# Optimization experiments

Hardware: AMD Instinct MI355X
Metric: run time of the kernel (lower is better)

## Reference

```python
import jax, jax.numpy as jnp
import numpy as np


def _pad_kernel_like(kernel_oc0, H, W, ks):
    # torch: F.pad(k,(p,p,p,p)) then if shape mismatch F.pad(k,(0,1,0,1))
    p = (H - ks) // 2
    extra = H - (ks + 2 * p)  # 0 or 1
    return jnp.pad(kernel_oc0, ((0, 0), (p, p + extra), (p, p + extra)))


def setup_inputs() -> dict:
    key = jax.random.key(0)
    k1, k2 = jax.random.split(key)
    B, C, H, W = 8, 16, 128, 128
    O, KS = 32, 9
    x = jax.random.normal(k1, (B, C, H, W), dtype=jnp.float32)
    # kaiming_uniform-ish init scale
    fan_in = C * KS * KS
    bound = float(np.sqrt(6.0 / fan_in))
    kernel = jax.random.uniform(k2, (O, C, KS, KS), dtype=jnp.float32,
                                minval=-bound, maxval=bound)
    return {"x": x, "kernel": kernel}


def reference(x, kernel):
    # x: [B,C,H,W] float32, kernel: [O,C,ks,ks] float32
    B, C, H, W = x.shape
    O, ks = kernel.shape[0], kernel.shape[-1]
    # Faithful to original bug: only kernel[:, 0] is used for every input channel.
    k = _pad_kernel_like(kernel[:, 0], H, W, ks)  # [O,H,W]
    # 4f optical FFT convolution: ifftshift -> FFT -> multiply -> IFFT -> fftshift -> |.|
    Fx = jnp.fft.fft2(jnp.fft.ifftshift(x, axes=(-2, -1)))   # [B,C,H,W] complex64
    Fk = jnp.fft.fft2(jnp.fft.ifftshift(k, axes=(-2, -1)))   # [O,H,W]   complex64
    prod = Fx[:, None, :, :, :] * Fk[None, :, None, :, :]    # [B,O,C,H,W]
    field = jnp.fft.fftshift(jnp.fft.ifft2(prod), axes=(-2, -1))
    out_pc = jnp.abs(field)                                  # per-(out,in)-channel intensity
    return out_pc.sum(axis=2)                                # [B,O,H,W]
```

## Files before the change

### kernel.cpp

```cpp
#include <hip/hip_runtime.h>


typedef __attribute__((ext_vector_type(8)))  short  short8;
typedef __attribute__((ext_vector_type(4)))  float  float4v;
typedef __attribute__((ext_vector_type(4)))  unsigned int uint4v;

#define NROW 10
#define NCC  144
#define CHSZ (NROW * NCC)
#define NSLOT (16 * NROW * 72)

__device__ __forceinline__ unsigned short f2bf(float f) {
    union { float f; unsigned int u; } a; a.f = f;
    unsigned int u = a.u;
    u += 0x7fffu + ((u >> 16) & 1u);
    return (unsigned short)(u >> 16);
}

#if __has_builtin(__builtin_amdgcn_alignbit)
#define ALIGN16(hi_, lo_) __builtin_amdgcn_alignbit((hi_), (lo_), 16)
#else
#define ALIGN16(hi_, lo_) \
    (unsigned int)((((unsigned long long)(hi_) << 32) | (lo_)) >> 16)
#endif

#define FRAG_EVEN(q_) __builtin_bit_cast(short8, (uint4v){                    \
        wnd[(q_)+0], wnd[(q_)+1], wnd[(q_)+2], wnd[(q_)+3]})
#define FRAG_ODD(q_)  __builtin_bit_cast(short8, (uint4v){                    \
        ALIGN16(wnd[(q_)+1], wnd[(q_)+0]),                                    \
        ALIGN16(wnd[(q_)+2], wnd[(q_)+1]),                                    \
        ALIGN16(wnd[(q_)+3], wnd[(q_)+2]),                                    \
        ALIGN16(wnd[(q_)+4], wnd[(q_)+3])})

#define LOAD_SLOT(s_, v0_, v1_, ad_)                                         \
    {                                                                        \
        int ch  = (s_) / 720;                                                \
        int rem = (s_) - 720 * ch;                                           \
        int rr  = rem / 72;                                                  \
        int ccd = rem - 72 * rr;                                             \
        int cc  = 2 * ccd;                                                   \
        int xrow = (i - 4 + rr) & 127;                                       \
        const float* xp = xb + (ch << 14) + (xrow << 7);                     \
        v0_ = xp[(132 - cc) & 127];                                          \
        v1_ = xp[(131 - cc) & 127];                                          \
        ad_ = ch * CHSZ + rr * NCC + cc;                                     \
    }

__global__ __launch_bounds__(512, 5)
void optical_conv_69698729279498(const float* __restrict__ x,
                                 const float* __restrict__ kern,
                                 float* __restrict__ out) {
    __shared__ __align__(16) unsigned short ldsb[16 * CHSZ];

    const int tid = threadIdx.x;
    const int l   = tid & 63;
    const int w   = tid >> 6;
    const int h   = w & 1;
    const int oh  = (w >> 1) & 1;
    const int cg  = w >> 2;
    const int i   = blockIdx.x;
    const int b   = blockIdx.y;

    const int lk   = l & 15;
    const int g    = (l >> 4) & 1;
    const int hi32 = l >> 5;
    const int g2   = l >> 4;
    const int o    = oh * 16 + lk;

    const float* xb = x + ((size_t)b << 18);

    float v0a[12], v1a[12]; int aa[12];
#pragma unroll
    for (int k = 0; k < 12; ++k) {
        int s = tid + 512 * k;
        LOAD_SLOT(s, v0a[k], v1a[k], aa[k]);
    }
    float v0b[11], v1b[11]; int ab[11];
#pragma unroll
    for (int k = 0; k < 11; ++k) {
        int s = tid + 512 * (12 + k);
        if (s > NSLOT - 1) s = NSLOT - 1;
        LOAD_SLOT(s, v0b[k], v1b[k], ab[k]);
    }
#pragma unroll
    for (int k = 0; k < 12; ++k) {
        unsigned int pk2 = (unsigned int)f2bf(v0a[k]) | ((unsigned int)f2bf(v1a[k]) << 16);
        *(unsigned int*)&ldsb[aa[k]] = pk2;
    }
#pragma unroll
    for (int k = 0; k < 11; ++k) {
        unsigned int pk2 = (unsigned int)f2bf(v0b[k]) | ((unsigned int)f2bf(v1b[k]) << 16);
        *(unsigned int*)&ldsb[ab[k]] = pk2;
    }

    short8 Bf[5];
#pragma unroll
    for (int ck = 0; ck < 5; ++ck) {
        const int ti  = 2 * ck + (g2 >> 1);
        const int tj0 = (g2 & 1) * 8;
        unsigned int pk[4];
#pragma unroll
        for (int ee = 0; ee < 4; ++ee) {
            int tj_a = tj0 + 2 * ee, tj_b = tj_a + 1;
            float va = (ti <= 8 && tj_a <= 8) ? kern[o * 1296 + ti * 9 + tj_a] : 0.f;
            float vb = (ti <= 8 && tj_b <= 8) ? kern[o * 1296 + ti * 9 + tj_b] : 0.f;
            pk[ee] = (unsigned int)f2bf(va) | ((unsigned int)f2bf(vb) << 16);
        }
        uint4v bv; bv.x = pk[0]; bv.y = pk[1]; bv.z = pk[2]; bv.w = pk[3];
        Bf[ck] = __builtin_bit_cast(short8, bv);
    }

    __syncthreads();

    float4v acc[4];
#pragma unroll
    for (int pp = 0; pp < 4; ++pp) acc[pp] = (float4v){0.f, 0.f, 0.f, 0.f};
    const float4v zero4 = (float4v){0.f, 0.f, 0.f, 0.f};

    const char* lb = (const char*)ldsb
                   + (240 - 16 * lk + 16 * g) + (1 - hi32) * 288
                   + cg * 8 * 2880;

    for (int c = 0; c < 8; ++c) {
        float4v D[4];
#pragma unroll
        for (int ck = 0; ck < 5; ++ck) {
            const char* p = lb + (8 - 2 * ck) * 288;
            uint4v w0 = *(const uint4v*)p;
            uint4v w1 = *(const uint4v*)(p + 16);
            unsigned int wnd[8] = {w0.x, w0.y, w0.z, w0.w, w1.x, w1.y, w1.z, w1.w};
            if (h == 0) {
                short8 f0 = FRAG_ODD(3),  f1 = FRAG_EVEN(3);
                short8 f2 = FRAG_ODD(2),  f3 = FRAG_EVEN(2);
                D[0] = __builtin_amdgcn_mfma_f32_16x16x32_bf16(f0, Bf[ck], ck ? D[0] : zero4, 0, 0, 0);
                D[1] = __builtin_amdgcn_mfma_f32_16x16x32_bf16(f1, Bf[ck], ck ? D[1] : zero4, 0, 0, 0);
                D[2] = __builtin_amdgcn_mfma_f32_16x16x32_bf16(f2, Bf[ck], ck ? D[2] : zero4, 0, 0, 0);
                D[3] = __builtin_amdgcn_mfma_f32_16x16x32_bf16(f3, Bf[ck], ck ? D[3] : zero4, 0, 0, 0);
            } else {
                short8 f0 = FRAG_ODD(1),  f1 = FRAG_EVEN(1);
                short8 f2 = FRAG_ODD(0),  f3 = FRAG_EVEN(0);
                D[0] = __builtin_amdgcn_mfma_f32_16x16x32_bf16(f0, Bf[ck], ck ? D[0] : zero4, 0, 0, 0);
                D[1] = __builtin_amdgcn_mfma_f32_16x16x32_bf16(f1, Bf[ck], ck ? D[1] : zero4, 0, 0, 0);
                D[2] = __builtin_amdgcn_mfma_f32_16x16x32_bf16(f2, Bf[ck], ck ? D[2] : zero4, 0, 0, 0);
                D[3] = __builtin_amdgcn_mfma_f32_16x16x32_bf16(f3, Bf[ck], ck ? D[3] : zero4, 0, 0, 0);
            }
        }
#pragma unroll
        for (int pp = 0; pp < 4; ++pp)
#pragma unroll
            for (int e = 0; e < 4; ++e) acc[pp][e] += fabsf(D[pp][e]);
        lb += 2880;
    }

    __syncthreads();
    float* red = (float*)ldsb;
    const int rbase = (((w & 3) << 6) + l) * 17;
    if (cg == 1) {
#pragma unroll
        for (int pp = 0; pp < 4; ++pp)
#pragma unroll
            for (int e = 0; e < 4; ++e) red[rbase + 4 * pp + e] = acc[pp][e];
    }
    __syncthreads();
    if (cg == 0) {
#pragma unroll
        for (int pp = 0; pp < 4; ++pp)
#pragma unroll
            for (int e = 0; e < 4; ++e) acc[pp][e] += red[rbase + 4 * pp + e];
        float* ob = out + ((((size_t)(b * 32 + o)) * 128 + i) << 7);
#pragma unroll
        for (int pp = 0; pp < 4; ++pp) {
            const int pprime = 4 * h + pp;
#pragma unroll
            for (int e = 0; e < 4; ++e)
                ob[32 * g2 + 8 * e + pprime] = acc[pp][e];
        }
    }
}

extern "C" void kernel_launch(void* const* d_in, const int* in_sizes, int n_in,
                              void* d_out, int out_size, void* d_ws, size_t ws_size,
                              hipStream_t stream) {
    const float* x = (const float*)d_in[0];
    const float* kern = (const float*)d_in[1];
    float* out = (float*)d_out;
    dim3 block(512);
    dim3 grid(128, 8);
    hipLaunchKernelGGL(optical_conv_69698729279498, grid, block, 0, stream,
                       x, kern, out);
}
```

Baseline: 106.9 us.

## Pre-convert input to padded bf16 workspace and DMA it into LDS

Adds a prep kernel that converts x to bf16 once, in a row-wrapped, column-reversed layout held in workspace, plus a tiny kernel that packs the kernel B-fragments. The main kernel then streams contiguous rows straight into LDS with global_load_lds instead of gathering floats and converting them per block. Each block now computes two output rows across all 16 channels, which removes the cross-wave LDS reduction and halves the grid. This trades redundant conversion and halo reloads for two extra launches and a workspace write and read pass.

```diff
diff --git a/kernel.cpp b/kernel.cpp
--- a/kernel.cpp
+++ b/kernel.cpp
@@ -5,16 +5,18 @@
 typedef __attribute__((ext_vector_type(4)))  float  float4v;
 typedef __attribute__((ext_vector_type(4)))  unsigned int uint4v;
 
-#define NROW 10
-#define NCC  144
-#define CHSZ (NROW * NCC)
-#define NSLOT (16 * NROW * 72)
+#define XR_ROWS 138
+#define XR_RDW  72
+#define XR_CH_DW (XR_ROWS * XR_RDW)
+#define XR_TOT_DW (128 * XR_CH_DW)
+#define BPRE_OFF ((size_t)128 * XR_ROWS * 288)
+#define CHB 3168
 
-__device__ __forceinline__ unsigned short f2bf(float f) {
+__device__ __forceinline__ unsigned int f2bf(float f) {
     union { float f; unsigned int u; } a; a.f = f;
     unsigned int u = a.u;
     u += 0x7fffu + ((u >> 16) & 1u);
-    return (unsigned short)(u >> 16);
+    return u >> 16;
 }
 
 #if __has_builtin(__builtin_amdgcn_alignbit)
@@ -32,33 +34,66 @@
         ALIGN16(wnd[(q_)+3], wnd[(q_)+2]),                                    \
         ALIGN16(wnd[(q_)+4], wnd[(q_)+3])})
 
-#define LOAD_SLOT(s_, v0_, v1_, ad_)                                         \
-    {                                                                        \
-        int ch  = (s_) / 720;                                                \
-        int rem = (s_) - 720 * ch;                                           \
-        int rr  = rem / 72;                                                  \
-        int ccd = rem - 72 * rr;                                             \
-        int cc  = 2 * ccd;                                                   \
-        int xrow = (i - 4 + rr) & 127;                                       \
-        const float* xp = xb + (ch << 14) + (xrow << 7);                     \
-        v0_ = xp[(132 - cc) & 127];                                          \
-        v1_ = xp[(131 - cc) & 127];                                          \
-        ad_ = ch * CHSZ + rr * NCC + cc;                                     \
+__device__ __forceinline__ void gload_lds16(const void* g, void* l) {
+    __builtin_amdgcn_global_load_lds(
+        (const __attribute__((address_space(1))) unsigned int*)g,
+        (__attribute__((address_space(3))) unsigned int*)l, 16, 0, 0);
+}
+
+__global__ __launch_bounds__(256)
+void optical_prep_x_69698729279498(const float* __restrict__ x,
+                                   unsigned int* __restrict__ xr) {
+    for (int idx = blockIdx.x * 256 + threadIdx.x; idx < XR_TOT_DW;
+         idx += gridDim.x * 256) {
+        int bc  = idx / XR_CH_DW;
+        int rem = idx - bc * XR_CH_DW;
+        int r   = rem / XR_RDW;
+        int ccd = rem - r * XR_RDW;
+        int cc  = 2 * ccd;
+        const float* xp = x + (bc << 14) + ((r & 127) << 7);
+        float v0 = xp[(132 - cc) & 127];
+        float v1 = xp[(131 - cc) & 127];
+        xr[idx] = f2bf(v0) | (f2bf(v1) << 16);
     }
+}
 
-__global__ __launch_bounds__(512, 5)
-void optical_conv_69698729279498(const float* __restrict__ x,
-                                 const float* __restrict__ kern,
+__global__ __launch_bounds__(64)
+void optical_prep_b_69698729279498(const float* __restrict__ kern,
+                                   uint4v* __restrict__ bpre) {
+    const int l  = threadIdx.x;
+    const int lk = l & 15;
+    const int g2 = l >> 4;
+    for (int oh = 0; oh < 2; ++oh) {
+        const int o = oh * 16 + lk;
+        for (int ck = 0; ck < 5; ++ck) {
+            const int ti  = 2 * ck + (g2 >> 1);
+            const int tj0 = (g2 & 1) * 8;
+            unsigned int pk[4];
+#pragma unroll
+            for (int ee = 0; ee < 4; ++ee) {
+                int tj_a = tj0 + 2 * ee, tj_b = tj_a + 1;
+                float va = (ti <= 8 && tj_a <= 8) ? kern[o * 1296 + ti * 9 + tj_a] : 0.f;
+                float vb = (ti <= 8 && tj_b <= 8) ? kern[o * 1296 + ti * 9 + tj_b] : 0.f;
+                pk[ee] = f2bf(va) | (f2bf(vb) << 16);
+            }
+            bpre[(oh * 5 + ck) * 64 + l] = (uint4v){pk[0], pk[1], pk[2], pk[3]};
+        }
+    }
+}
+
+__global__ __launch_bounds__(512, 4)
+void optical_conv_69698729279498(const unsigned int* __restrict__ xr,
+                                 const uint4v* __restrict__ bpre,
                                  float* __restrict__ out) {
-    __shared__ __align__(16) unsigned short ldsb[16 * CHSZ];
+    __shared__ __align__(16) unsigned short ldsb[16 * (CHB / 2)];
 
     const int tid = threadIdx.x;
     const int l   = tid & 63;
     const int w   = tid >> 6;
     const int h   = w & 1;
     const int oh  = (w >> 1) & 1;
-    const int cg  = w >> 2;
-    const int i   = blockIdx.x;
+    const int rh  = w >> 2;
+    const int i0  = blockIdx.x * 2;
     const int b   = blockIdx.y;
 
     const int lk   = l & 15;
@@ -67,48 +102,24 @@
     const int g2   = l >> 4;
     const int o    = oh * 16 + lk;
 
-    const float* xb = x + ((size_t)b << 18);
-
-    float v0a[12], v1a[12]; int aa[12];
+    const int wstart = (i0 >= 4) ? (i0 - 4) : (i0 + 124);
+    const char* xr8 = (const char*)xr;
 #pragma unroll
-    for (int k = 0; k < 12; ++k) {
-        int s = tid + 512 * k;
-        LOAD_SLOT(s, v0a[k], v1a[k], aa[k]);
-    }
-    float v0b[11], v1b[11]; int ab[11];
-#pragma unroll
-    for (int k = 0; k < 11; ++k) {
-        int s = tid + 512 * (12 + k);
-        if (s > NSLOT - 1) s = NSLOT - 1;
-        LOAD_SLOT(s, v0b[k], v1b[k], ab[k]);
-    }
-#pragma unroll
-    for (int k = 0; k < 12; ++k) {
-        unsigned int pk2 = (unsigned int)f2bf(v0a[k]) | ((unsigned int)f2bf(v1a[k]) << 16);
-        *(unsigned int*)&ldsb[aa[k]] = pk2;
-    }
-#pragma unroll
-    for (int k = 0; k < 11; ++k) {
-        unsigned int pk2 = (unsigned int)f2bf(v0b[k]) | ((unsigned int)f2bf(v1b[k]) << 16);
-        *(unsigned int*)&ldsb[ab[k]] = pk2;
+    for (int cw = 0; cw < 2; ++cw) {
+        const int ch = 2 * w + cw;
+        const char* src = xr8 + ((size_t)((b * 16 + ch) * XR_ROWS + wstart)) * 288;
+        char* dst = (char*)ldsb + ch * CHB;
+        gload_lds16(src + 0 * 1024 + l * 16, dst + 0 * 1024);
+        gload_lds16(src + 1 * 1024 + l * 16, dst + 1 * 1024);
+        gload_lds16(src + 2 * 1024 + l * 16, dst + 2 * 1024);
+        if (l < 6)
+            gload_lds16(src + 3072 + l * 16, dst + 3072);
     }
 
     short8 Bf[5];
 #pragma unroll
-    for (int ck = 0; ck < 5; ++ck) {
-        const int ti  = 2 * ck + (g2 >> 1);
-        const int tj0 = (g2 & 1) * 8;
-        unsigned int pk[4];
-#pragma unroll
-        for (int ee = 0; ee < 4; ++ee) {
-            int tj_a = tj0 + 2 * ee, tj_b = tj_a + 1;
-            float va = (ti <= 8 && tj_a <= 8) ? kern[o * 1296 + ti * 9 + tj_a] : 0.f;
-            float vb = (ti <= 8 && tj_b <= 8) ? kern[o * 1296 + ti * 9 + tj_b] : 0.f;
-            pk[ee] = (unsigned int)f2bf(va) | ((unsigned int)f2bf(vb) << 16);
-        }
-        uint4v bv; bv.x = pk[0]; bv.y = pk[1]; bv.z = pk[2]; bv.w = pk[3];
-        Bf[ck] = __builtin_bit_cast(short8, bv);
-    }
+    for (int ck = 0; ck < 5; ++ck)
+        Bf[ck] = __builtin_bit_cast(short8, bpre[(oh * 5 + ck) * 64 + l]);
 
     __syncthreads();
 
@@ -118,10 +129,9 @@
     const float4v zero4 = (float4v){0.f, 0.f, 0.f, 0.f};
 
     const char* lb = (const char*)ldsb
-                   + (240 - 16 * lk + 16 * g) + (1 - hi32) * 288
-                   + cg * 8 * 2880;
+                   + (240 - 16 * lk + 16 * g) + (1 - hi32 + rh) * 288;
 
-    for (int c = 0; c < 8; ++c) {
+    for (int c = 0; c < 16; ++c) {
         float4v D[4];
 #pragma unroll
         for (int ck = 0; ck < 5; ++ck) {
@@ -149,32 +159,17 @@
         for (int pp = 0; pp < 4; ++pp)
 #pragma unroll
             for (int e = 0; e < 4; ++e) acc[pp][e] += fabsf(D[pp][e]);
-        lb += 2880;
+        lb += CHB;
     }
 
-    __syncthreads();
-    float* red = (float*)ldsb;
-    const int rbase = (((w & 3) << 6) + l) * 17;
-    if (cg == 1) {
+    const int i = i0 + rh;
+    float* ob = out + ((((size_t)(b * 32 + o)) * 128 + i) << 7);
 #pragma unroll
-        for (int pp = 0; pp < 4; ++pp)
+    for (int pp = 0; pp < 4; ++pp) {
+        const int pprime = 4 * h + pp;
 #pragma unroll
-            for (int e = 0; e < 4; ++e) red[rbase + 4 * pp + e] = acc[pp][e];
-    }
-    __syncthreads();
-    if (cg == 0) {
-#pragma unroll
-        for (int pp = 0; pp < 4; ++pp)
-#pragma unroll
-            for (int e = 0; e < 4; ++e) acc[pp][e] += red[rbase + 4 * pp + e];
-        float* ob = out + ((((size_t)(b * 32 + o)) * 128 + i) << 7);
-#pragma unroll
-        for (int pp = 0; pp < 4; ++pp) {
-            const int pprime = 4 * h + pp;
-#pragma unroll
-            for (int e = 0; e < 4; ++e)
-                ob[32 * g2 + 8 * e + pprime] = acc[pp][e];
-        }
+        for (int e = 0; e < 4; ++e)
+            ob[32 * g2 + 8 * e + pprime] = acc[pp][e];
     }
 }
 
@@ -184,8 +179,13 @@
     const float* x = (const float*)d_in[0];
     const float* kern = (const float*)d_in[1];
     float* out = (float*)d_out;
-    dim3 block(512);
-    dim3 grid(128, 8);
-    hipLaunchKernelGGL(optical_conv_69698729279498, grid, block, 0, stream,
-                       x, kern, out);
+    unsigned int* xr = (unsigned int*)d_ws;
+    uint4v* bpre = (uint4v*)((char*)d_ws + BPRE_OFF);
+
+    hipLaunchKernelGGL(optical_prep_x_69698729279498, dim3(4096), dim3(256),
+                       0, stream, x, xr);
+    hipLaunchKernelGGL(optical_prep_b_69698729279498, dim3(1), dim3(64),
+                       0, stream, kern, bpre);
+    hipLaunchKernelGGL(optical_conv_69698729279498, dim3(64, 8), dim3(512),
+                       0, stream, xr, bpre, out);
 }
```

New measurement: 99.55 us. 6.9% less time.
